# Optimization experiments

Hardware: AMD Instinct MI355X
Metric: run time of the kernel (lower is better)

Reference implementation:

```python
import jax, jax.numpy as jnp
import numpy as np

B, T, C = 4, 2048, 768
NH, NKV, HD = 12, 12, 64
RMS_EPS = 1e-6


def rms_norm(x):
    return x * jax.lax.rsqrt(jnp.mean(x * x, axis=-1, keepdims=True) + RMS_EPS)


def apply_rotary_emb(x, cos, sin):
    # x: [B,T,H,D], cos/sin: [T,D/2]
    d2 = x.shape[-1] // 2
    x1, x2 = x[..., :d2], x[..., d2:]
    c = cos[None, :, None, :]
    s = sin[None, :, None, :]
    return jnp.concatenate([x1 * c - x2 * s, x1 * s + x2 * c], axis=-1)


def setup_inputs() -> dict:
    key = jax.random.key(0)
    ks = jax.random.split(key, 10)
    inv_freq = 1.0 / (100000.0 ** (np.arange(0, HD, 2, dtype=np.float32) / HD))  # [HD/2]
    t = np.arange(T, dtype=np.float32)
    freqs = np.outer(t, inv_freq)  # [T, HD/2]
    return {
        "x": jax.random.normal(ks[0], (B, T, C), jnp.float32),
        "ve": jax.random.normal(ks[1], (B, T, C), jnp.float32),
        "cos": jnp.asarray(np.cos(freqs)),
        "sin": jnp.asarray(np.sin(freqs)),
        "Wq": jax.random.normal(ks[2], (C, C), jnp.float32) * (1.0 / np.sqrt(C)),
        "Wk": jax.random.normal(ks[3], (C, C), jnp.float32) * (1.0 / np.sqrt(C)),
        "Wv": jax.random.normal(ks[4], (C, C), jnp.float32) * (1.0 / np.sqrt(C)),
        "Wproj": jax.random.normal(ks[5], (C, C), jnp.float32) * (1.0 / np.sqrt(C)),
        "Wgate": jax.random.normal(ks[6], (NKV, 12), jnp.float32) * 0.1,
        "window_left": 1024,
    }


def reference(x, ve, cos, sin, Wq, Wk, Wv, Wproj, Wgate, window_left):
    q = (x @ Wq.T).reshape(B, T, NH, HD)
    k = (x @ Wk.T).reshape(B, T, NKV, HD)
    v = (x @ Wv.T).reshape(B, T, NKV, HD)

    # value-embedding gating (has_ve path): gate = 3*sigmoid(Linear(x[...,:12]))
    ve_h = ve.reshape(B, T, NKV, HD)
    gate = 3.0 * jax.nn.sigmoid(x[..., :12] @ Wgate.T)  # [B,T,NKV]
    v = v + gate[..., None] * ve_h

    q = apply_rotary_emb(q, cos, sin)
    k = apply_rotary_emb(k, cos, sin)
    q = rms_norm(q) * 1.2
    k = rms_norm(k) * 1.2

    # sliding-window causal bias
    row = jnp.arange(T)[:, None]
    col = jnp.arange(T)[None, :]
    mask = (row >= col) & ((row - col) <= window_left)
    bias = jnp.where(mask, 0.0, -1e9).astype(x.dtype)  # [T,T]

    scale = 1.0 / np.sqrt(HD)
    att = jnp.einsum("bqhd,bkhd->bhqk", q, k) * scale + bias[None, None]
    att = jax.nn.softmax(att, axis=-1)
    y = jnp.einsum("bhqk,bkhd->bqhd", att, v).reshape(B, T, C)
    return y @ Wproj.T
```

## Files before the change

kernel.cpp:

```cpp
#include <hip/hip_runtime.h>
#include <hip/hip_bf16.h>
#include <cstdint>
#include <cstddef>

#define B_  4
#define T_  2048
#define C_  768
#define NH_ 12
#define HD_ 64

typedef __bf16 bf16_t;
typedef __attribute__((ext_vector_type(8))) __bf16 bf16x8;
typedef __attribute__((ext_vector_type(4))) __bf16 bf16x4;
typedef __attribute__((ext_vector_type(4))) float floatx4;
typedef __attribute__((ext_vector_type(8))) unsigned short ushort8;

#define MFMA16(a, b, c) __builtin_amdgcn_mfma_f32_16x16x32_bf16((a), (b), (c), 0, 0, 0)

#define SM_C1 0.18033688f
#define SM_C2 -17.3123405f

typedef const __attribute__((address_space(1))) uint8_t* gptr_t;
typedef __attribute__((address_space(3))) uint8_t* lptr_t;

static __device__ __forceinline__ void gld16(const void* g, void* l) {
    __builtin_amdgcn_global_load_lds((gptr_t)g, (lptr_t)l, 16, 0, 0);
}

static __device__ __forceinline__ float bfl(unsigned p) {
    return __builtin_bit_cast(float, p << 16);
}
static __device__ __forceinline__ float bfh(unsigned p) {
    return __builtin_bit_cast(float, p & 0xffff0000u);
}

__global__ __launch_bounds__(256) void cvt_all_kernel(
    const void* s0, const void* s1, const void* s2, const void* s3,
    const void* s4, const void* s5, const void* s6, const void* s7, const void* s8,
    bf16_t* d0, bf16_t* d1, bf16_t* d2, bf16_t* d3,
    bf16_t* d4, bf16_t* d5, bf16_t* d6, bf16_t* d7, bf16_t* d8)
{
    const bool isf32 = (((const unsigned short*)s2)[0] == 0);
    if (!isf32) return;
    const void* srcs[9] = {s0, s1, s2, s3, s4, s5, s6, s7, s8};
    bf16_t*     dsts[9] = {d0, d1, d2, d3, d4, d5, d6, d7, d8};
    const int   ns[9]   = {B_*T_*C_, B_*T_*C_, T_*32, T_*32,
                           C_*C_, C_*C_, C_*C_, C_*C_, 144};
    const int t = blockIdx.y;
    const float* sf = (const float*)srcs[t];
    bf16_t*     dst = dsts[t];
    const int   nc  = ns[t] >> 3;
    const int stride = gridDim.x * 256;
    for (int i = blockIdx.x * 256 + threadIdx.x; i < nc; i += stride) {
        ushort8 o;
#pragma unroll
        for (int j = 0; j < 8; j++)
            o[j] = (unsigned short)__builtin_bit_cast(unsigned short,
                     (bf16_t)sf[i * 8 + j]);
        *(ushort8*)&dst[i * 8] = o;
    }
}

__global__ __launch_bounds__(256, 3) void gemm_qkv_fused(
    const void* xr,  const bf16_t* xc,
    const void* wqr, const bf16_t* wqc,
    const void* wkr, const bf16_t* wkc,
    const void* wvr, const bf16_t* wvc,
    const void* cr,  const bf16_t* ccv,
    const void* sr,  const bf16_t* scv,
    const void* ver, const bf16_t* vec,
    const void* wgr, const bf16_t* wgc,
    bf16_t* qn, bf16_t* kn, bf16_t* vt)
{
    __shared__ alignas(16) char sm[36864];
    const bool f32 = (((const unsigned short*)cr)[0] == 0);
    const bf16_t* X  = f32 ? xc  : (const bf16_t*)xr;
    const bf16_t* WQ = f32 ? wqc : (const bf16_t*)wqr;
    const bf16_t* WK = f32 ? wkc : (const bf16_t*)wkr;
    const bf16_t* WV = f32 ? wvc : (const bf16_t*)wvr;
    const bf16_t* CC = f32 ? ccv : (const bf16_t*)cr;
    const bf16_t* SS = f32 ? scv : (const bf16_t*)sr;
    const bf16_t* VE = f32 ? vec : (const bf16_t*)ver;
    const bf16_t* WG = f32 ? wgc : (const bf16_t*)wgr;

    const int sel = blockIdx.y / 6;
    const int nt  = blockIdx.y % 6;
    const int m0  = blockIdx.x * 128;
    const int n0  = nt * 128;
    const bf16_t* Bm = (sel == 0) ? WQ : (sel == 1) ? WK : WV;

    bf16_t* As = (bf16_t*)sm;
    bf16_t* Bs = (bf16_t*)(sm + 16384);

    const int tid  = threadIdx.x;
    const int lane = tid & 63;
    const int wid  = tid >> 6;
    const int m16  = lane & 15;
    const int quad = lane >> 4;
    const int wm   = (wid >> 1) * 64;
    const int wn   = (wid & 1) * 64;
    const int srow = lane >> 2;
    const int soct = (lane & 3) * 8;

    floatx4 acc[4][4];
#pragma unroll
    for (int i = 0; i < 4; i++)
#pragma unroll
        for (int j = 0; j < 4; j++) acc[i][j] = (floatx4){0.f, 0.f, 0.f, 0.f};

    for (int k0 = 0; k0 < C_; k0 += 64) {
        const bf16_t* ga0 = &X[(size_t)(m0 + 16 * wid + srow) * C_ + k0 + soct];
        const bf16_t* gb0 = &Bm[(size_t)(n0 + 16 * wid + srow) * C_ + k0 + soct];
        gld16(ga0,                        As + wid * 512);
        gld16(ga0 + (size_t)64 * C_,      As + wid * 512 + 2048);
        gld16(gb0,                        Bs + wid * 512);
        gld16(gb0 + (size_t)64 * C_,      Bs + wid * 512 + 2048);
        gld16(ga0 + 32,                   As + 4096 + wid * 512);
        gld16(ga0 + (size_t)64 * C_ + 32, As + 4096 + wid * 512 + 2048);
        gld16(gb0 + 32,                   Bs + 4096 + wid * 512);
        gld16(gb0 + (size_t)64 * C_ + 32, Bs + 4096 + wid * 512 + 2048);
        __syncthreads();
#pragma unroll
        for (int half = 0; half < 2; half++) {
            bf16x8 af[4], bfr[4];
#pragma unroll
            for (int i = 0; i < 4; i++)
                af[i] = *(const bf16x8*)&As[half * 4096 + (wm + i * 16 + m16) * 32 + quad * 8];
#pragma unroll
            for (int j = 0; j < 4; j++)
                bfr[j] = *(const bf16x8*)&Bs[half * 4096 + (wn + j * 16 + m16) * 32 + quad * 8];
#pragma unroll
            for (int i = 0; i < 4; i++)
#pragma unroll
                for (int j = 0; j < 4; j++)
                    acc[i][j] = MFMA16(af[i], bfr[j], acc[i][j]);
        }
        __syncthreads();
    }

    if (sel < 2) {
        unsigned* csT = (unsigned*)sm;
        const int tbase = m0 & 2047;
        for (int idx = tid; idx < 128 * 32; idx += 256) {
            const int rr = idx >> 5, dd = idx & 31;
            const unsigned cv = ((const unsigned short*)CC)[(tbase + rr) * 32 + dd];
            const unsigned sv = ((const unsigned short*)SS)[(tbase + rr) * 32 + dd];
            csT[rr * 33 + dd] = cv | (sv << 16);
        }
        __syncthreads();
        bf16_t* OUT = (sel == 0) ? qn : kn;
#pragma unroll
        for (int i = 0; i < 4; i++) {
            float c0[4], s0[4], c1[4], s1[4];
#pragma unroll
            for (int r = 0; r < 4; r++) {
                const int rl = wm + i * 16 + quad * 4 + r;
                const unsigned p0 = csT[rl * 33 + m16];
                const unsigned p1 = csT[rl * 33 + 16 + m16];
                c0[r] = bfl(p0); s0[r] = bfh(p0);
                c1[r] = bfl(p1); s1[r] = bfh(p1);
            }
            floatx4 r0, r1, r2, r3;
            float ss[4];
#pragma unroll
            for (int r = 0; r < 4; r++) {
                r0[r] = acc[i][0][r] * c0[r] - acc[i][2][r] * s0[r];
                r1[r] = acc[i][1][r] * c1[r] - acc[i][3][r] * s1[r];
                r2[r] = acc[i][0][r] * s0[r] + acc[i][2][r] * c0[r];
                r3[r] = acc[i][1][r] * s1[r] + acc[i][3][r] * c1[r];
                ss[r] = r0[r]*r0[r] + r1[r]*r1[r] + r2[r]*r2[r] + r3[r]*r3[r];
            }
#pragma unroll
            for (int r = 0; r < 4; r++) {
#pragma unroll
                for (int off = 1; off < 16; off <<= 1)
                    ss[r] += __shfl_xor(ss[r], off, 64);
            }
#pragma unroll
            for (int r = 0; r < 4; r++) {
                const float scl = rsqrtf(ss[r] * (1.f / 64.f) + 1e-6f) * 1.2f;
                const size_t rowoff = (size_t)(m0 + wm + i * 16 + quad * 4 + r) * C_
                                      + n0 + wn + m16;
                OUT[rowoff]      = (bf16_t)(r0[r] * scl);
                OUT[rowoff + 16] = (bf16_t)(r1[r] * scl);
                OUT[rowoff + 32] = (bf16_t)(r2[r] * scl);
                OUT[rowoff + 48] = (bf16_t)(r3[r] * scl);
            }
        }
    } else {
        bf16_t* veT = (bf16_t*)sm;
        float*  gT  = (float*)(sm + 34816);
        for (int idx = tid; idx < 2048; idx += 256) {
            const int rr = idx >> 4, ch = idx & 15;
            *(bf16x8*)&veT[rr * 136 + ch * 8] =
                *(const bf16x8*)&VE[(size_t)(m0 + rr) * C_ + n0 + ch * 8];
        }
        {
            const int row = tid & 127, hh = tid >> 7;
            const int head = nt * 2 + hh;
            float g = 0.f;
#pragma unroll
            for (int j2 = 0; j2 < 12; j2++)
                g += (float)X[(size_t)(m0 + row) * C_ + j2] * (float)WG[head * 12 + j2];
            gT[hh * 128 + row] = 3.f / (1.f + __expf(-g));
        }
        __syncthreads();
        const int hh2  = wn >> 6;
        const int head = nt * 2 + hh2;
        const int bb = m0 >> 11, t0 = m0 & 2047;
#pragma unroll
        for (int i = 0; i < 4; i++) {
            const floatx4 gr = *(const floatx4*)&gT[hh2 * 128 + wm + i * 16 + quad * 4];
            const int tslot = t0 + wm + (i >> 1) * 32 + quad * 8 + (i & 1) * 4;
#pragma unroll
            for (int j = 0; j < 4; j++) {
                bf16x4 o;
#pragma unroll
                for (int r = 0; r < 4; r++) {
                    const float vef = (float)veT[(wm + i * 16 + quad * 4 + r) * 136
                                                 + wn + j * 16 + m16];
                    o[r] = (bf16_t)(acc[i][j][r] + gr[r] * vef);
                }
                *(bf16x4*)&vt[((size_t)(bb * NH_ + head) * HD_ + j * 16 + m16) * T_
                              + tslot] = o;
            }
        }
    }
}

template <bool OUT_BF16>
__device__ __forceinline__ void gemm_bt_tile(
    const bf16_t* __restrict__ A, const bf16_t* __restrict__ Bm,
    void* __restrict__ Cout, int m0, int n0, int K, int ldc)
{
    __shared__ bf16_t As[2][128 * 32];
    __shared__ bf16_t Bs[2][128 * 32];
    const int tid  = threadIdx.x;
    const int lane = tid & 63;
    const int wid  = tid >> 6;
    const int m16  = lane & 15;
    const int quad = lane >> 4;
    const int wm   = (wid >> 1) * 64;
    const int wn   = (wid & 1) * 64;
    const int srow = lane >> 2;
    const int soct = (lane & 3) * 8;

    floatx4 acc[4][4];
#pragma unroll
    for (int i = 0; i < 4; i++)
#pragma unroll
        for (int j = 0; j < 4; j++) acc[i][j] = (floatx4){0.f, 0.f, 0.f, 0.f};

    for (int k0 = 0; k0 < K; k0 += 64) {
        const bf16_t* ga0 = &A[(size_t)(m0 + 16 * wid + srow) * K + k0 + soct];
        const bf16_t* gb0 = &Bm[(size_t)(n0 + 16 * wid + srow) * K + k0 + soct];
        gld16(ga0,                       (bf16_t*)As[0] + wid * 512);
        gld16(ga0 + (size_t)64 * K,      (bf16_t*)As[0] + wid * 512 + 2048);
        gld16(gb0,                       (bf16_t*)Bs[0] + wid * 512);
        gld16(gb0 + (size_t)64 * K,      (bf16_t*)Bs[0] + wid * 512 + 2048);
        gld16(ga0 + 32,                  (bf16_t*)As[1] + wid * 512);
        gld16(ga0 + (size_t)64 * K + 32, (bf16_t*)As[1] + wid * 512 + 2048);
        gld16(gb0 + 32,                  (bf16_t*)Bs[1] + wid * 512);
        gld16(gb0 + (size_t)64 * K + 32, (bf16_t*)Bs[1] + wid * 512 + 2048);
        __syncthreads();
#pragma unroll
        for (int half = 0; half < 2; half++) {
            bf16x8 af[4], bfr[4];
#pragma unroll
            for (int i = 0; i < 4; i++)
                af[i] = *(const bf16x8*)&As[half][(wm + i * 16 + m16) * 32 + quad * 8];
#pragma unroll
            for (int j = 0; j < 4; j++)
                bfr[j] = *(const bf16x8*)&Bs[half][(wn + j * 16 + m16) * 32 + quad * 8];
#pragma unroll
            for (int i = 0; i < 4; i++)
#pragma unroll
                for (int j = 0; j < 4; j++)
                    acc[i][j] = MFMA16(af[i], bfr[j], acc[i][j]);
        }
        __syncthreads();
    }
#pragma unroll
    for (int i = 0; i < 4; i++) {
#pragma unroll
        for (int j = 0; j < 4; j++) {
            const int colg = n0 + wn + j * 16 + m16;
#pragma unroll
            for (int r = 0; r < 4; r++) {
                const int rowg = m0 + wm + i * 16 + quad * 4 + r;
                if (OUT_BF16)
                    ((bf16_t*)Cout)[(size_t)rowg * ldc + colg] = (bf16_t)acc[i][j][r];
                else
                    ((float*)Cout)[(size_t)rowg * ldc + colg] = acc[i][j][r];
            }
        }
    }
}

__global__ __launch_bounds__(256, 3) void gemm_proj_kernel(
    const bf16_t* __restrict__ yb, const void* wpr, const bf16_t* wpc,
    void* __restrict__ out, const void* cr)
{
    const bool f32 = (((const unsigned short*)cr)[0] == 0);
    const bf16_t* WP = f32 ? wpc : (const bf16_t*)wpr;
    if (f32)
        gemm_bt_tile<false>(yb, WP, out, blockIdx.x * 128, blockIdx.y * 128, C_, C_);
    else
        gemm_bt_tile<true>(yb, WP, out, blockIdx.x * 128, blockIdx.y * 128, C_, C_);
}

__global__ __launch_bounds__(256, 3) void attn_kernel(
    const bf16_t* __restrict__ Q, const bf16_t* __restrict__ Km,
    const bf16_t* __restrict__ Vtg, bf16_t* __restrict__ Y,
    const int* __restrict__ wl)
{
    const int bx   = blockIdx.x;
    const int bh   = blockIdx.y;
    const int gsel = bh >> 4;
    int qblk;
    if (gsel == 0)      qblk = bx;
    else if (gsel == 1) qblk = 15 - bx;
    else                qblk = (int)((0xECA8642013579BDFull >> (bx * 4)) & 0xF);
    const int q0 = qblk * 128;
    const int b  = bh / NH_;
    const int h  = bh % NH_;
    const int window = wl[0];
    const int tid  = threadIdx.x;
    const int wid  = tid >> 6;
    const int lane = tid & 63;
    const int m16  = lane & 15;
    const int quad = lane >> 4;
    const int qw   = q0 + wid * 32;

    const bf16_t* Qb = Q + (size_t)b * T_ * C_ + h * HD_;
    const bf16_t* Kb = Km + (size_t)b * T_ * C_ + h * HD_;
    const bf16_t* Vb = Vtg + (size_t)bh * HD_ * T_;

    __shared__ bf16_t Ks[2][64 * 64];
    __shared__ bf16_t Vs[2][64 * 64];

    bf16x8 qf[2][2];
#pragma unroll
    for (int mt = 0; mt < 2; mt++)
#pragma unroll
        for (int ks = 0; ks < 2; ks++)
            qf[mt][ks] = *(const bf16x8*)
                &Qb[(size_t)(qw + mt * 16 + m16) * C_ + ks * 32 + quad * 8];

    const int srow = tid >> 2;
    const int soct = tid & 3;
    const int g0   = 2 * soct, g1 = 2 * soct + 1;
    const int kd0  = srow * 64 + ((g0 ^ (srow & 7)) << 3);
    const int kd1  = srow * 64 + ((g1 ^ (srow & 7)) << 3);
    int rsw[2];
#pragma unroll
    for (int ks = 0; ks < 2; ks++)
        rsw[ks] = (((ks * 4 + quad) ^ (m16 & 7)) << 3);

    int lo = q0 - window;
    if (lo < 0) lo = 0;
    lo &= ~63;
    const int nch = (q0 + 128 - lo) >> 6;

    floatx4 accO[2][4];
#pragma unroll
    for (int mt = 0; mt < 2; mt++)
#pragma unroll
        for (int dt = 0; dt < 4; dt++) accO[mt][dt] = (floatx4){0.f, 0.f, 0.f, 0.f};
    float lsum[2] = {0.f, 0.f};
    const bf16x4 zero4 = {(bf16_t)0.f, (bf16_t)0.f, (bf16_t)0.f, (bf16_t)0.f};

    bf16x8 ka0 = *(const bf16x8*)&Kb[(size_t)(lo + srow) * C_ + g0 * 8];
    bf16x8 ka1 = *(const bf16x8*)&Kb[(size_t)(lo + srow) * C_ + g1 * 8];
    bf16x8 va0 = *(const bf16x8*)&Vb[(size_t)srow * T_ + lo + g0 * 8];
    bf16x8 va1 = *(const bf16x8*)&Vb[(size_t)srow * T_ + lo + g1 * 8];
    *(bf16x8*)&Ks[0][kd0] = ka0;
    *(bf16x8*)&Ks[0][kd1] = ka1;
    *(bf16x8*)&Vs[0][kd0] = va0;
    *(bf16x8*)&Vs[0][kd1] = va1;

    for (int ic = 0; ic < nch; ic++) {
        const int kc = lo + ic * 64;
        const bool more = (ic + 1 < nch);
        if (more) {
            const int kn2 = kc + 64;
            ka0 = *(const bf16x8*)&Kb[(size_t)(kn2 + srow) * C_ + g0 * 8];
            ka1 = *(const bf16x8*)&Kb[(size_t)(kn2 + srow) * C_ + g1 * 8];
            va0 = *(const bf16x8*)&Vb[(size_t)srow * T_ + kn2 + g0 * 8];
            va1 = *(const bf16x8*)&Vb[(size_t)srow * T_ + kn2 + g1 * 8];
        }
        __syncthreads();
        const int buf = ic & 1;

        const bool skip = (kc > qw + 31) || (kc + 63 < qw - window);
        if (!skip) {
            bf16x8 kf[4][2];
#pragma unroll
            for (int nt = 0; nt < 4; nt++) {
                const int rb = (nt * 16 + m16) * 64;
                kf[nt][0] = *(const bf16x8*)&Ks[buf][rb + rsw[0]];
                kf[nt][1] = *(const bf16x8*)&Ks[buf][rb + rsw[1]];
            }
            bf16x4 pk[2][4];
            unsigned livemask = 0;
#pragma unroll
            for (int mt = 0; mt < 2; mt++) {
                const int qmin = qw + mt * 16, qmax = qmin + 15;
                float lacc = 0.f;
#pragma unroll
                for (int nt = 0; nt < 4; nt++) {
                    const int kmin = kc + nt * 16, kmax = kmin + 15;
                    if (kmin > qmax || kmax < qmin - window) {
                        pk[mt][nt] = zero4;
                        continue;
                    }
                    livemask |= 1u << (mt * 4 + nt);
                    floatx4 z = (floatx4){0.f, 0.f, 0.f, 0.f};
                    z = MFMA16(kf[nt][0], qf[mt][0], z);
                    z = MFMA16(kf[nt][1], qf[mt][1], z);
                    const bool edge = (kmax > qmin) || (kmin < qmax - window);
                    const int query = qmin + m16;
                    bf16x4 t4;
#pragma unroll
                    for (int r = 0; r < 4; r++) {
                        float p = __builtin_amdgcn_exp2f(
                            fmaf(z[r], SM_C1, SM_C2));
                        if (edge) {
                            const int key = kmin + quad * 4 + r;
                            const bool ok = (key <= query) &&
                                            (query - key <= window);
                            p = ok ? p : 0.f;
                        }
                        t4[r] = (bf16_t)p;
                        lacc += p;
                    }
                    pk[mt][nt] = t4;
                }
                lsum[mt] += lacc;
            }
#pragma unroll
            for (int pr = 0; pr < 2; pr++) {
                const unsigned pm0 = (livemask >> (2 * pr)) & 3u;
                const unsigned pm1 = (livemask >> (4 + 2 * pr)) & 3u;
                if (!(pm0 | pm1)) continue;
                const bf16x8 pa0 = __builtin_shufflevector(
                    pk[0][2 * pr], pk[0][2 * pr + 1], 0, 1, 2, 3, 4, 5, 6, 7);
                const bf16x8 pa1 = __builtin_shufflevector(
                    pk[1][2 * pr], pk[1][2 * pr + 1], 0, 1, 2, 3, 4, 5, 6, 7);
                const int vco = (((pr * 4 + quad) ^ (m16 & 7)) << 3);
#pragma unroll
                for (int dt = 0; dt < 4; dt++) {
                    const bf16x8 vf = *(const bf16x8*)
                        &Vs[buf][(dt * 16 + m16) * 64 + vco];
                    if (pm0) accO[0][dt] = MFMA16(pa0, vf, accO[0][dt]);
                    if (pm1) accO[1][dt] = MFMA16(pa1, vf, accO[1][dt]);
                }
            }
        }

        if (more) {
            const int nb = buf ^ 1;
            *(bf16x8*)&Ks[nb][kd0] = ka0;
            *(bf16x8*)&Ks[nb][kd1] = ka1;
            *(bf16x8*)&Vs[nb][kd0] = va0;
            *(bf16x8*)&Vs[nb][kd1] = va1;
        }
    }

#pragma unroll
    for (int mt = 0; mt < 2; mt++) {
        float red = lsum[mt];
        red += __shfl_xor(red, 16, 64);
        red += __shfl_xor(red, 32, 64);
#pragma unroll
        for (int r = 0; r < 4; r++) {
            const float lq  = __shfl(red, quad * 4 + r, 64);
            const float inv = 1.f / lq;
            const int   tq  = qw + mt * 16 + quad * 4 + r;
#pragma unroll
            for (int dt = 0; dt < 4; dt++)
                Y[((size_t)b * T_ + tq) * C_ + h * HD_ + dt * 16 + m16] =
                    (bf16_t)(accO[mt][dt][r] * inv);
        }
    }
}

extern "C" void kernel_launch(void* const* d_in, const int* in_sizes, int n_in,
                              void* d_out, int out_size, void* d_ws, size_t ws_size,
                              hipStream_t stream)
{
    const void* x_raw   = d_in[0];
    const void* ve_raw  = d_in[1];
    const void* cos_raw = d_in[2];
    const void* sin_raw = d_in[3];
    const void* wq_raw  = d_in[4];
    const void* wk_raw  = d_in[5];
    const void* wv_raw  = d_in[6];
    const void* wp_raw  = d_in[7];
    const void* wg_raw  = d_in[8];
    const int*  wl      = (const int*)d_in[9];

    const size_t NTC = (size_t)B_ * T_ * C_;
    const size_t WSZ = (size_t)C_ * C_;

    bf16_t* ws  = (bf16_t*)d_ws;
    bf16_t* xb  = ws;
    bf16_t* veb = xb + NTC;
    bf16_t* cb  = veb + NTC;
    bf16_t* sb  = cb + T_ * 32;
    bf16_t* wqb = sb + T_ * 32;
    bf16_t* wkb = wqb + WSZ;
    bf16_t* wvb = wkb + WSZ;
    bf16_t* wpb = wvb + WSZ;
    bf16_t* wgb = wpb + WSZ;
    bf16_t* qn  = wgb + 256;
    bf16_t* kn  = qn + NTC;
    bf16_t* vt  = kn + NTC;
    bf16_t* yb  = vt + NTC;

    cvt_all_kernel<<<dim3(128, 9), 256, 0, stream>>>(
        x_raw, ve_raw, cos_raw, sin_raw, wq_raw, wk_raw, wv_raw, wp_raw, wg_raw,
        xb, veb, cb, sb, wqb, wkb, wvb, wpb, wgb);

    gemm_qkv_fused<<<dim3(64, 18), 256, 0, stream>>>(
        x_raw, xb, wq_raw, wqb, wk_raw, wkb, wv_raw, wvb,
        cos_raw, cb, sin_raw, sb, ve_raw, veb, wg_raw, wgb,
        qn, kn, vt);

    attn_kernel<<<dim3(16, 48), 256, 0, stream>>>(qn, kn, vt, yb, wl);

    gemm_proj_kernel<<<dim3(64, 6), 256, 0, stream>>>(yb, wp_raw, wpb, d_out, cos_raw);
}
```

Measured before the change: 234.6 us.

## Make attention single-wave blocks reading K/V directly from global memory

Rewrites the attention kernel so each 64-thread block handles one 32-query slice and loads K and V fragments straight from global memory, dropping the shared-memory double buffer and block barriers. The grid becomes 48x64 with a rotated query-block mapping to spread causal work across blocks. This removes LDS staging and __syncthreads cost and shrinks each block to its own key range, but gives up K/V sharing across four waves, so cache and global traffic rise and V reads become strided.

```diff
diff --git a/kernel.cpp b/kernel.cpp
--- a/kernel.cpp
+++ b/kernel.cpp
@@ -309,36 +309,24 @@
         gemm_bt_tile<true>(yb, WP, out, blockIdx.x * 128, blockIdx.y * 128, C_, C_);
 }
 
-__global__ __launch_bounds__(256, 3) void attn_kernel(
+__global__ __launch_bounds__(64, 4) void attn_kernel(
     const bf16_t* __restrict__ Q, const bf16_t* __restrict__ Km,
     const bf16_t* __restrict__ Vtg, bf16_t* __restrict__ Y,
     const int* __restrict__ wl)
 {
-    const int bx   = blockIdx.x;
-    const int bh   = blockIdx.y;
-    const int gsel = bh >> 4;
-    int qblk;
-    if (gsel == 0)      qblk = bx;
-    else if (gsel == 1) qblk = 15 - bx;
-    else                qblk = (int)((0xECA8642013579BDFull >> (bx * 4)) & 0xF);
-    const int q0 = qblk * 128;
+    const int bh = blockIdx.x;
+    const int qw = (int)((blockIdx.y + blockIdx.x) & 63) * 32;
     const int b  = bh / NH_;
     const int h  = bh % NH_;
     const int window = wl[0];
-    const int tid  = threadIdx.x;
-    const int wid  = tid >> 6;
-    const int lane = tid & 63;
+    const int lane = threadIdx.x & 63;
     const int m16  = lane & 15;
     const int quad = lane >> 4;
-    const int qw   = q0 + wid * 32;
 
     const bf16_t* Qb = Q + (size_t)b * T_ * C_ + h * HD_;
     const bf16_t* Kb = Km + (size_t)b * T_ * C_ + h * HD_;
     const bf16_t* Vb = Vtg + (size_t)bh * HD_ * T_;
 
-    __shared__ bf16_t Ks[2][64 * 64];
-    __shared__ bf16_t Vs[2][64 * 64];
-
     bf16x8 qf[2][2];
 #pragma unroll
     for (int mt = 0; mt < 2; mt++)
@@ -347,20 +335,10 @@
             qf[mt][ks] = *(const bf16x8*)
                 &Qb[(size_t)(qw + mt * 16 + m16) * C_ + ks * 32 + quad * 8];
 
-    const int srow = tid >> 2;
-    const int soct = tid & 3;
-    const int g0   = 2 * soct, g1 = 2 * soct + 1;
-    const int kd0  = srow * 64 + ((g0 ^ (srow & 7)) << 3);
-    const int kd1  = srow * 64 + ((g1 ^ (srow & 7)) << 3);
-    int rsw[2];
-#pragma unroll
-    for (int ks = 0; ks < 2; ks++)
-        rsw[ks] = (((ks * 4 + quad) ^ (m16 & 7)) << 3);
-
-    int lo = q0 - window;
+    int lo = qw - window;
     if (lo < 0) lo = 0;
     lo &= ~63;
-    const int nch = (q0 + 128 - lo) >> 6;
+    const int nch = ((qw + 31 - lo) >> 6) + 1;
 
     floatx4 accO[2][4];
 #pragma unroll
@@ -370,100 +348,73 @@
     float lsum[2] = {0.f, 0.f};
     const bf16x4 zero4 = {(bf16_t)0.f, (bf16_t)0.f, (bf16_t)0.f, (bf16_t)0.f};
 
-    bf16x8 ka0 = *(const bf16x8*)&Kb[(size_t)(lo + srow) * C_ + g0 * 8];
-    bf16x8 ka1 = *(const bf16x8*)&Kb[(size_t)(lo + srow) * C_ + g1 * 8];
-    bf16x8 va0 = *(const bf16x8*)&Vb[(size_t)srow * T_ + lo + g0 * 8];
-    bf16x8 va1 = *(const bf16x8*)&Vb[(size_t)srow * T_ + lo + g1 * 8];
-    *(bf16x8*)&Ks[0][kd0] = ka0;
-    *(bf16x8*)&Ks[0][kd1] = ka1;
-    *(bf16x8*)&Vs[0][kd0] = va0;
-    *(bf16x8*)&Vs[0][kd1] = va1;
-
     for (int ic = 0; ic < nch; ic++) {
         const int kc = lo + ic * 64;
-        const bool more = (ic + 1 < nch);
-        if (more) {
-            const int kn2 = kc + 64;
-            ka0 = *(const bf16x8*)&Kb[(size_t)(kn2 + srow) * C_ + g0 * 8];
-            ka1 = *(const bf16x8*)&Kb[(size_t)(kn2 + srow) * C_ + g1 * 8];
-            va0 = *(const bf16x8*)&Vb[(size_t)srow * T_ + kn2 + g0 * 8];
-            va1 = *(const bf16x8*)&Vb[(size_t)srow * T_ + kn2 + g1 * 8];
-        }
-        __syncthreads();
-        const int buf = ic & 1;
-
-        const bool skip = (kc > qw + 31) || (kc + 63 < qw - window);
-        if (!skip) {
-            bf16x8 kf[4][2];
+
+        bf16x8 kf[4][2];
+#pragma unroll
+        for (int nt = 0; nt < 4; nt++) {
+            const bf16_t* kr = &Kb[(size_t)(kc + nt * 16 + m16) * C_];
+#pragma unroll
+            for (int ks = 0; ks < 2; ks++)
+                kf[nt][ks] = *(const bf16x8*)&kr[ks * 32 + quad * 8];
+        }
+
+        bf16x4 pk[2][4];
+        unsigned livemask = 0;
+#pragma unroll
+        for (int mt = 0; mt < 2; mt++) {
+            const int qmin = qw + mt * 16, qmax = qmin + 15;
+            float lacc = 0.f;
 #pragma unroll
             for (int nt = 0; nt < 4; nt++) {
-                const int rb = (nt * 16 + m16) * 64;
-                kf[nt][0] = *(const bf16x8*)&Ks[buf][rb + rsw[0]];
-                kf[nt][1] = *(const bf16x8*)&Ks[buf][rb + rsw[1]];
-            }
-            bf16x4 pk[2][4];
-            unsigned livemask = 0;
-#pragma unroll
-            for (int mt = 0; mt < 2; mt++) {
-                const int qmin = qw + mt * 16, qmax = qmin + 15;
-                float lacc = 0.f;
-#pragma unroll
-                for (int nt = 0; nt < 4; nt++) {
-                    const int kmin = kc + nt * 16, kmax = kmin + 15;
-                    if (kmin > qmax || kmax < qmin - window) {
-                        pk[mt][nt] = zero4;
-                        continue;
+                const int kmin = kc + nt * 16, kmax = kmin + 15;
+                if (kmin > qmax || kmax < qmin - window) {
+                    pk[mt][nt] = zero4;
+                    continue;
+                }
+                livemask |= 1u << (mt * 4 + nt);
+                floatx4 z = (floatx4){0.f, 0.f, 0.f, 0.f};
+                z = MFMA16(kf[nt][0], qf[mt][0], z);
+                z = MFMA16(kf[nt][1], qf[mt][1], z);
+                const bool edge = (kmax > qmin) || (kmin < qmax - window);
+                const int query = qmin + m16;
+                bf16x4 t4;
+#pragma unroll
+                for (int r = 0; r < 4; r++) {
+                    float p = __builtin_amdgcn_exp2f(
+                        fmaf(z[r], SM_C1, SM_C2));
+                    if (edge) {
+                        const int key = kmin + quad * 4 + r;
+                        const bool ok = (key <= query) &&
+                                        (query - key <= window);
+                        p = ok ? p : 0.f;
                     }
-                    livemask |= 1u << (mt * 4 + nt);
-                    floatx4 z = (floatx4){0.f, 0.f, 0.f, 0.f};
-                    z = MFMA16(kf[nt][0], qf[mt][0], z);
-                    z = MFMA16(kf[nt][1], qf[mt][1], z);
-                    const bool edge = (kmax > qmin) || (kmin < qmax - window);
-                    const int query = qmin + m16;
-                    bf16x4 t4;
-#pragma unroll
-                    for (int r = 0; r < 4; r++) {
-                        float p = __builtin_amdgcn_exp2f(
-                            fmaf(z[r], SM_C1, SM_C2));
-                        if (edge) {
-                            const int key = kmin + quad * 4 + r;
-                            const bool ok = (key <= query) &&
-                                            (query - key <= window);
-                            p = ok ? p : 0.f;
-                        }
-                        t4[r] = (bf16_t)p;
-                        lacc += p;
-                    }
-                    pk[mt][nt] = t4;
+                    t4[r] = (bf16_t)p;
+                    lacc += p;
                 }
-                lsum[mt] += lacc;
-            }
-#pragma unroll
-            for (int pr = 0; pr < 2; pr++) {
-                const unsigned pm0 = (livemask >> (2 * pr)) & 3u;
-                const unsigned pm1 = (livemask >> (4 + 2 * pr)) & 3u;
-                if (!(pm0 | pm1)) continue;
-                const bf16x8 pa0 = __builtin_shufflevector(
-                    pk[0][2 * pr], pk[0][2 * pr + 1], 0, 1, 2, 3, 4, 5, 6, 7);
-                const bf16x8 pa1 = __builtin_shufflevector(
-                    pk[1][2 * pr], pk[1][2 * pr + 1], 0, 1, 2, 3, 4, 5, 6, 7);
-                const int vco = (((pr * 4 + quad) ^ (m16 & 7)) << 3);
-#pragma unroll
-                for (int dt = 0; dt < 4; dt++) {
-                    const bf16x8 vf = *(const bf16x8*)
-                        &Vs[buf][(dt * 16 + m16) * 64 + vco];
-                    if (pm0) accO[0][dt] = MFMA16(pa0, vf, accO[0][dt]);
-                    if (pm1) accO[1][dt] = MFMA16(pa1, vf, accO[1][dt]);
-                }
-            }
-        }
-
-        if (more) {
-            const int nb = buf ^ 1;
-            *(bf16x8*)&Ks[nb][kd0] = ka0;
-            *(bf16x8*)&Ks[nb][kd1] = ka1;
-            *(bf16x8*)&Vs[nb][kd0] = va0;
-            *(bf16x8*)&Vs[nb][kd1] = va1;
+                pk[mt][nt] = t4;
+            }
+            lsum[mt] += lacc;
+        }
+
+#pragma unroll
+        for (int pr = 0; pr < 2; pr++) {
+            const unsigned pm0 = (livemask >> (2 * pr)) & 3u;
+            const unsigned pm1 = (livemask >> (4 + 2 * pr)) & 3u;
+            if (!(pm0 | pm1)) continue;
+            const bf16x8 pa0 = __builtin_shufflevector(
+                pk[0][2 * pr], pk[0][2 * pr + 1], 0, 1, 2, 3, 4, 5, 6, 7);
+            const bf16x8 pa1 = __builtin_shufflevector(
+                pk[1][2 * pr], pk[1][2 * pr + 1], 0, 1, 2, 3, 4, 5, 6, 7);
+            const int vcol = kc + (pr * 4 + quad) * 8;
+#pragma unroll
+            for (int dt = 0; dt < 4; dt++) {
+                const bf16x8 vf = *(const bf16x8*)
+                    &Vb[(size_t)(dt * 16 + m16) * T_ + vcol];
+                if (pm0) accO[0][dt] = MFMA16(pa0, vf, accO[0][dt]);
+                if (pm1) accO[1][dt] = MFMA16(pa1, vf, accO[1][dt]);
+            }
         }
     }
 
@@ -527,7 +478,7 @@
         cos_raw, cb, sin_raw, sb, ve_raw, veb, wg_raw, wgb,
         qn, kn, vt);
 
-    attn_kernel<<<dim3(16, 48), 256, 0, stream>>>(qn, kn, vt, yb, wl);
+    attn_kernel<<<dim3(48, 64), 64, 0, stream>>>(qn, kn, vt, yb, wl);
 
     gemm_proj_kernel<<<dim3(64, 6), 256, 0, stream>>>(yb, wp_raw, wpb, d_out, cos_raw);
 }
```

Result: slower. 261.1 us (+11.3%).
